# Kernel tuning notes

Measured on AMD Instinct MI355X. Metric: run time of the kernel, lower is better.

## Reference

```python
import jax, jax.numpy as jnp
import numpy as np

B, L, D = 4, 4096, 1024


def setup_inputs() -> dict:
    key = jax.random.key(0)
    ks = jax.random.split(key, 10)
    s = 1.0 / np.sqrt(D)  # torch Linear default init scale
    return {
        "x": jax.random.normal(ks[0], (B, L, D), dtype=jnp.float32),
        "hidden": jax.random.normal(ks[1], (B, D), dtype=jnp.float32),
        "W_ln_z": jax.random.uniform(ks[2], (D, D), jnp.float32, -s, s),
        "b_ln_z": jax.random.uniform(ks[3], (D,), jnp.float32, -s, s),
        "W_dt": jax.random.uniform(ks[4], (D, D), jnp.float32, -s, s),
        "b_dt": jax.random.uniform(ks[5], (D,), jnp.float32, -s, s),
        "W_y": jax.random.uniform(ks[6], (D, D), jnp.float32, -s, s),
        "b_y": jax.random.uniform(ks[7], (D,), jnp.float32, -s, s),
        "W_g": jax.random.uniform(ks[8], (D, D), jnp.float32, -s, s),
        "b_g": jax.random.uniform(ks[9], (D,), jnp.float32, -s, s),
    }


def reference(x, hidden, W_ln_z, b_ln_z, W_dt, b_dt, W_y, b_y, W_g, b_g):
    # Linear projections (torch Linear: x @ W.T + b)
    z_pre = x @ W_ln_z.T + b_ln_z          # (B, L, D)
    dt_pre = x @ W_dt.T + b_dt             # (B, L, D)

    # -softplus(-u) == log_sigmoid(u)
    ln_z = jax.nn.log_sigmoid(z_pre)       # ln z
    ln_da = jax.nn.log_sigmoid(dt_pre)     # ln(delta*a)
    ln_z_da = ln_z + ln_da
    ln_o_da = jax.nn.log_sigmoid(-dt_pre)  # -softplus(dt_pre)

    ln_o_da_cumsum = jnp.cumsum(ln_o_da, axis=1)
    # log-space parallel scan: h_t = sum_{s<=t} z_s*da_s * prod_{s<r<=t} o_da_r
    lcse = jax.lax.cumlogsumexp(ln_z_da - ln_o_da_cumsum, axis=1)
    h_inner = jnp.exp(lcse + ln_o_da_cumsum)                       # (B, L, D)
    h_cross = jnp.exp(ln_o_da_cumsum) * hidden[:, None, :]         # (B, L, D)
    h = h_inner + h_cross

    gate = jax.nn.silu(x @ W_g.T + b_g)
    y = (h @ W_y.T + b_y) * gate
    return y, h
```

## Files before the change

kernel.cpp:

```cpp
#include <hip/hip_runtime.h>


#define BDIM 4
#define LDIM 4096
#define DDIM 1024
#define MROWS (BDIM * LDIM)
#define KDIM 1024
#define NPROJ 3072
#define NCHUNK 64
#define LCHUNK 64

typedef __attribute__((ext_vector_type(8))) short short8v;
typedef __attribute__((ext_vector_type(4))) float f32x4;

__device__ __forceinline__ float bf2f(short u) {
    union { float f; unsigned int i; } v;
    v.i = ((unsigned int)(unsigned short)u) << 16;
    return v.f;
}
__device__ __forceinline__ short f2bf(float f) {
    union { float f; unsigned int i; } v; v.f = f;
    unsigned int r = v.i + 0x7FFFu + ((v.i >> 16) & 1u);
    return (short)(r >> 16);
}
__device__ __forceinline__ float sigf(float x) { return 1.f / (1.f + __expf(-x)); }

__global__ void cast_f32_bf16(const float* __restrict__ src, short* __restrict__ dst, int n4) {
    int i = blockIdx.x * blockDim.x + threadIdx.x;
    int stride = gridDim.x * blockDim.x;
    for (; i < n4; i += stride) {
        float4 v = reinterpret_cast<const float4*>(src)[i];
        short4 o;
        o.x = f2bf(v.x); o.y = f2bf(v.y); o.z = f2bf(v.z); o.w = f2bf(v.w);
        reinterpret_cast<short4*>(dst)[i] = o;
    }
}

__global__ void cast4_f32_bf16(const float* __restrict__ s0, const float* __restrict__ s1,
                               const float* __restrict__ s2, const float* __restrict__ s3,
                               short* __restrict__ dst) {
    int i = blockIdx.x * blockDim.x + threadIdx.x;
    int seg = i >> 18, off = i & ((1 << 18) - 1);
    const float* s = (seg == 0) ? s0 : (seg == 1) ? s1 : (seg == 2) ? s2 : s3;
    float4 v = reinterpret_cast<const float4*>(s)[off];
    short4 o;
    o.x = f2bf(v.x); o.y = f2bf(v.y); o.z = f2bf(v.z); o.w = f2bf(v.w);
    reinterpret_cast<short4*>(dst)[i] = o;
}


#define STAGE(arr, gbase, half, kofs)                                              \
  do {                                                                             \
    _Pragma("unroll")                                                              \
    for (int _i = 0; _i < 2; ++_i) {                                               \
      int _c = _i * 512 + tid;                                                     \
      int _row = _c >> 3, _g = _c & 7;                                             \
      int _gsw = _g ^ (_row & 7);                                                  \
      __builtin_amdgcn_global_load_lds(                                            \
        (const __attribute__((address_space(1))) void*)(                           \
            (gbase) + (size_t)((half) * 128 + _row) * K + (kofs) + _gsw * 8),      \
        (__attribute__((address_space(3))) void*)(                                 \
            &arr[(_i * 512 + wid * 64) * 8]),                                      \
        16, 0, 0);                                                                 \
    }                                                                              \
  } while (0)

#define LDA4(dst, arr)                                                             \
  _Pragma("unroll")                                                                \
  for (int _m = 0; _m < 4; ++_m) {                                                 \
    int _r = _m * 32 + wm * 16 + lrow;                                             \
    _Pragma("unroll")                                                              \
    for (int _kk = 0; _kk < 2; ++_kk)                                              \
      dst[_m][_kk] = *(const short8v*)&arr[_r * 64 +                               \
                       (((_kk * 4 + kq) ^ (lrow & 7)) * 8)];                       \
  }

#define LDB2(dst, arr)                                                             \
  _Pragma("unroll")                                                                \
  for (int _n = 0; _n < 2; ++_n) {                                                 \
    int _r = _n * 64 + wn * 16 + lrow;                                             \
    _Pragma("unroll")                                                              \
    for (int _kk = 0; _kk < 2; ++_kk)                                              \
      dst[_n][_kk] = *(const short8v*)&arr[_r * 64 +                               \
                       (((_kk * 4 + kq) ^ (lrow & 7)) * 8)];                       \
  }

#define MFMAQ(mi0, ni0, afr, bfr)                                                  \
  __builtin_amdgcn_s_setprio(1);                                                   \
  _Pragma("unroll")                                                                \
  for (int _kk = 0; _kk < 2; ++_kk)                                                \
    _Pragma("unroll")                                                              \
    for (int _m = 0; _m < 4; ++_m)                                                 \
      _Pragma("unroll")                                                            \
      for (int _n = 0; _n < 2; ++_n)                                               \
        acc[(mi0) + _m][(ni0) + _n] = __builtin_amdgcn_mfma_f32_16x16x32_bf16(     \
            afr[_m][_kk], bfr[_n][_kk], acc[(mi0) + _m][(ni0) + _n], 0, 0, 0);     \
  __builtin_amdgcn_s_setprio(0);

#define BARB()       __builtin_amdgcn_s_barrier()
#define BAR_VM4()    asm volatile("s_waitcnt vmcnt(4)\ns_barrier" ::: "memory")
#define BAR_VM0()    asm volatile("s_waitcnt vmcnt(0)\ns_barrier" ::: "memory")

template<int OUT_BF16, int HAS_GATE>
__global__ __launch_bounds__(512, 2) void gemm256(
    const short* __restrict__ A, const short* __restrict__ Bm,
    const float* __restrict__ bias, void* __restrict__ Cv,
    int M, int N, int K,
    const short* __restrict__ gate, int ldg)
{
    __shared__ short As0h0[8192], As0h1[8192], As1h0[8192], As1h1[8192];
    __shared__ short Bs0h0[8192], Bs0h1[8192], Bs1h0[8192], Bs1h1[8192];

    const int tid  = threadIdx.x;
    const int lane = tid & 63;
    const int wid  = tid >> 6;
    const int wm   = wid >> 2;
    const int wn   = wid & 3;
    const int lrow = lane & 15;
    const int kq   = lane >> 4;

    const int gx  = gridDim.x;
    const int nwg = gx * gridDim.y;
    int flat = blockIdx.y * gx + blockIdx.x;
    if ((nwg & 7) == 0) { int q = nwg >> 3; flat = (flat & 7) * q + (flat >> 3); }
    const int m0 = (flat / gx) * 256;
    const int n0 = (flat % gx) * 256;

    const short* Abase = A + (size_t)m0 * K;
    const short* Bbase = Bm + (size_t)n0 * K;

    f32x4 acc[8][4];
#pragma unroll
    for (int i = 0; i < 8; ++i)
#pragma unroll
        for (int j = 0; j < 4; ++j)
            acc[i][j] = (f32x4){0.f, 0.f, 0.f, 0.f};

    STAGE(As0h0, Abase, 0, 0);
    STAGE(As0h1, Abase, 1, 0);
    STAGE(Bs0h0, Bbase, 0, 0);
    STAGE(Bs0h1, Bbase, 1, 0);
    STAGE(As1h0, Abase, 0, 64);
    STAGE(Bs1h0, Bbase, 0, 64);
    BAR_VM4();

    const int NT = K / 64;
    for (int t = 0; t < NT; t += 2) {
        const int k1 = (t + 1) * 64, k2 = (t + 2) * 64, k3 = (t + 3) * 64;
        const bool more = (t + 2) < NT;
        short8v af[4][2], b0[2][2], b1[2][2];

        LDA4(af, As0h0) LDB2(b0, Bs0h0) LDB2(b1, Bs0h1)
        STAGE(As1h1, Abase, 1, k1);
        STAGE(Bs1h1, Bbase, 1, k1);
        BARB(); MFMAQ(0, 0, af, b0) MFMAQ(0, 2, af, b1) BARB();

        LDA4(af, As0h1)
        if (more) { STAGE(As0h0, Abase, 0, k2); STAGE(Bs0h0, Bbase, 0, k2); }
        BARB(); MFMAQ(4, 2, af, b1) MFMAQ(4, 0, af, b0)
        if (more) { BAR_VM4(); } else { BAR_VM0(); }

        LDA4(af, As1h0) LDB2(b0, Bs1h0) LDB2(b1, Bs1h1)
        if (more) { STAGE(As0h1, Abase, 1, k2); STAGE(Bs0h1, Bbase, 1, k2); }
        BARB(); MFMAQ(0, 0, af, b0) MFMAQ(0, 2, af, b1) BARB();

        LDA4(af, As1h1)
        if (more) { STAGE(As1h0, Abase, 0, k3); STAGE(Bs1h0, Bbase, 0, k3); }
        BARB(); MFMAQ(4, 2, af, b1) MFMAQ(4, 0, af, b0)
        if (more) { BAR_VM4(); } else { BARB(); }
    }

    const int lr4 = (lane >> 4) * 4;
#pragma unroll
    for (int mi = 0; mi < 8; ++mi) {
        int rowb = m0 + mi * 32 + wm * 16 + lr4;
#pragma unroll
        for (int ni = 0; ni < 4; ++ni) {
            int col = n0 + ni * 64 + wn * 16 + lrow;
            float bv = bias[col];
#pragma unroll
            for (int r = 0; r < 4; ++r) {
                int row = rowb + r;
                float val = acc[mi][ni][r] + bv;
                if (HAS_GATE) {
                    float g = bf2f(gate[(size_t)row * ldg + col]);
                    val *= g * sigf(g);
                }
                if (OUT_BF16)
                    ((short*)Cv)[(size_t)row * N + col] = f2bf(val);
                else
                    ((float*)Cv)[(size_t)row * N + col] = val;
            }
        }
    }
}

__global__ __launch_bounds__(1024) void chunk_reduce(
    const short* __restrict__ pre, float* __restrict__ sA, float* __restrict__ sBv)
{
    const int d = threadIdx.x;
    const int c = blockIdx.x;
    const int b = blockIdx.y;
    float Aacc = 1.f, Bacc = 0.f;
    size_t base = ((size_t)(b * LDIM) + c * LCHUNK) * NPROJ;
    for (int i = 0; i < LCHUNK; ++i) {
        float z  = bf2f(pre[base + d]);
        float dt = bf2f(pre[base + DDIM + d]);
        float e  = __expf(-dt);
        float r  = 1.f / (1.f + e);
        float oda = e * r;
        float zda = sigf(z) * r;
        Bacc = zda + oda * Bacc;
        Aacc *= oda;
        base += NPROJ;
    }
    int idx = ((b * NCHUNK + c) << 10) + d;
    sA[idx]  = Aacc;
    sBv[idx] = Bacc;
}

__global__ __launch_bounds__(1024) void chunk_prefix(
    const float* __restrict__ sA, const float* __restrict__ sBv,
    const float* __restrict__ hidden, float* __restrict__ sI)
{
    const int d = threadIdx.x;
    const int b = blockIdx.x;
    float h = hidden[b * DDIM + d];
    for (int c = 0; c < NCHUNK; ++c) {
        int idx = ((b * NCHUNK + c) << 10) + d;
        sI[idx] = h;
        h = sBv[idx] + sA[idx] * h;
    }
}

__global__ __launch_bounds__(1024) void chunk_apply(
    const short* __restrict__ pre, const float* __restrict__ sI,
    float* __restrict__ hout, short* __restrict__ hbf)
{
    const int d = threadIdx.x;
    const int c = blockIdx.x;
    const int b = blockIdx.y;
    float h = sI[((b * NCHUNK + c) << 10) + d];
    size_t base  = ((size_t)(b * LDIM) + c * LCHUNK) * NPROJ;
    size_t obase = ((size_t)(b * LDIM) + c * LCHUNK) * DDIM + d;
    for (int i = 0; i < LCHUNK; ++i) {
        float z  = bf2f(pre[base + d]);
        float dt = bf2f(pre[base + DDIM + d]);
        float e  = __expf(-dt);
        float r  = 1.f / (1.f + e);
        float oda = e * r;
        float zda = sigf(z) * r;
        h = zda + oda * h;
        hout[obase] = h;
        hbf[obase]  = f2bf(h);
        base += NPROJ;
        obase += DDIM;
    }
}

extern "C" void kernel_launch(void* const* d_in, const int* in_sizes, int n_in,
                              void* d_out, int out_size, void* d_ws, size_t ws_size,
                              hipStream_t stream) {
    const float* x      = (const float*)d_in[0];
    const float* hidden = (const float*)d_in[1];
    const float* W_ln_z = (const float*)d_in[2];
    const float* b_ln_z = (const float*)d_in[3];
    const float* W_dt   = (const float*)d_in[4];
    const float* b_dt   = (const float*)d_in[5];
    const float* W_y    = (const float*)d_in[6];
    const float* b_y    = (const float*)d_in[7];
    const float* W_g    = (const float*)d_in[8];
    const float* b_g    = (const float*)d_in[9];

    char* ws = (char*)d_ws;
    short* x_bf   = (short*)(ws + 0);
    short* Wcat   = (short*)(ws + 33554432);
    short* Wy_bf  = (short*)(ws + 39845888);
    float* biascat= (float*)(ws + 41943040);
    short* pre    = (short*)(ws + 41955328);
    float* sA     = (float*)(ws + 142618624);
    float* sBv    = (float*)(ws + 143667200);
    float* sI     = (float*)(ws + 144715776);

    cast_f32_bf16<<<2048, 256, 0, stream>>>(x, x_bf, (MROWS * KDIM) / 4);
    cast4_f32_bf16<<<4096, 256, 0, stream>>>(W_ln_z, W_dt, W_g, W_y, Wcat);

    hipMemcpyAsync(biascat,            b_ln_z, DDIM * sizeof(float), hipMemcpyDeviceToDevice, stream);
    hipMemcpyAsync(biascat + DDIM,     b_dt,   DDIM * sizeof(float), hipMemcpyDeviceToDevice, stream);
    hipMemcpyAsync(biascat + 2 * DDIM, b_g,    DDIM * sizeof(float), hipMemcpyDeviceToDevice, stream);

    gemm256<1, 0><<<dim3(NPROJ / 256, MROWS / 256), 512, 0, stream>>>(
        x_bf, Wcat, biascat, pre, MROWS, NPROJ, KDIM, nullptr, 0);

    float* y_out = (float*)d_out;
    float* h_out = (float*)d_out + (size_t)MROWS * DDIM;
    short* h_bf  = x_bf;
    chunk_reduce<<<dim3(NCHUNK, BDIM), 1024, 0, stream>>>(pre, sA, sBv);
    chunk_prefix<<<dim3(BDIM), 1024, 0, stream>>>(sA, sBv, hidden, sI);
    chunk_apply<<<dim3(NCHUNK, BDIM), 1024, 0, stream>>>(pre, sI, h_out, h_bf);

    gemm256<0, 1><<<dim3(DDIM / 256, MROWS / 256), 512, 0, stream>>>(
        h_bf, Wy_bf, b_y, y_out, MROWS, DDIM, KDIM, pre + 2 * DDIM, NPROJ);
}
```

Baseline: 281.1 us.

## Split GEMM phases into finer LDS/MFMA interleave and pack scan kernel elements

The GEMM main loop is split into eight smaller phases, each pairing one LDS fragment load and one global stage with a single MFMA quarter, separated by barriers. The vmcnt waits are issued separately from the barriers so global loads can overlap more MFMA work. Separately, the chunked scan kernels now process two channels per thread with 32-bit bf16 pair loads and float2 stores, halving the thread count. This adds barriers per iteration, and the scan kernels launch fewer threads, which lowers parallelism on an already small grid.

```diff
diff --git a/kernel.cpp b/kernel.cpp
--- a/kernel.cpp
+++ b/kernel.cpp
@@ -97,9 +97,9 @@
             afr[_m][_kk], bfr[_n][_kk], acc[(mi0) + _m][(ni0) + _n], 0, 0, 0);     \
   __builtin_amdgcn_s_setprio(0);
 
-#define BARB()       __builtin_amdgcn_s_barrier()
-#define BAR_VM4()    asm volatile("s_waitcnt vmcnt(4)\ns_barrier" ::: "memory")
-#define BAR_VM0()    asm volatile("s_waitcnt vmcnt(0)\ns_barrier" ::: "memory")
+#define BARB()   __builtin_amdgcn_s_barrier()
+#define VM4()    asm volatile("s_waitcnt vmcnt(4)")
+#define VM0()    asm volatile("s_waitcnt vmcnt(0)")
 
 template<int OUT_BF16, int HAS_GATE>
 __global__ __launch_bounds__(512, 2) void gemm256(
@@ -142,7 +142,7 @@
     STAGE(Bs0h1, Bbase, 1, 0);
     STAGE(As1h0, Abase, 0, 64);
     STAGE(Bs1h0, Bbase, 0, 64);
-    BAR_VM4();
+    VM4(); BARB();
 
     const int NT = K / 64;
     for (int t = 0; t < NT; t += 2) {
@@ -150,24 +150,35 @@
         const bool more = (t + 2) < NT;
         short8v af[4][2], b0[2][2], b1[2][2];
 
-        LDA4(af, As0h0) LDB2(b0, Bs0h0) LDB2(b1, Bs0h1)
+        LDA4(af, As0h0) LDB2(b0, Bs0h0)
         STAGE(As1h1, Abase, 1, k1);
+        BARB(); MFMAQ(0, 0, af, b0)
+
+        LDB2(b1, Bs0h1)
         STAGE(Bs1h1, Bbase, 1, k1);
-        BARB(); MFMAQ(0, 0, af, b0) MFMAQ(0, 2, af, b1) BARB();
+        BARB(); MFMAQ(0, 2, af, b1)
 
         LDA4(af, As0h1)
-        if (more) { STAGE(As0h0, Abase, 0, k2); STAGE(Bs0h0, Bbase, 0, k2); }
-        BARB(); MFMAQ(4, 2, af, b1) MFMAQ(4, 0, af, b0)
-        if (more) { BAR_VM4(); } else { BAR_VM0(); }
-
-        LDA4(af, As1h0) LDB2(b0, Bs1h0) LDB2(b1, Bs1h1)
-        if (more) { STAGE(As0h1, Abase, 1, k2); STAGE(Bs0h1, Bbase, 1, k2); }
-        BARB(); MFMAQ(0, 0, af, b0) MFMAQ(0, 2, af, b1) BARB();
+        if (more) STAGE(As0h0, Abase, 0, k2);
+        BARB(); MFMAQ(4, 2, af, b1)
+
+        if (more) { STAGE(Bs0h0, Bbase, 0, k2); VM4(); } else { VM0(); }
+        BARB(); MFMAQ(4, 0, af, b0)
+
+        LDA4(af, As1h0) LDB2(b0, Bs1h0)
+        if (more) STAGE(As0h1, Abase, 1, k2);
+        BARB(); MFMAQ(0, 0, af, b0)
+
+        LDB2(b1, Bs1h1)
+        if (more) STAGE(Bs0h1, Bbase, 1, k2);
+        BARB(); MFMAQ(0, 2, af, b1)
 
         LDA4(af, As1h1)
-        if (more) { STAGE(As1h0, Abase, 0, k3); STAGE(Bs1h0, Bbase, 0, k3); }
-        BARB(); MFMAQ(4, 2, af, b1) MFMAQ(4, 0, af, b0)
-        if (more) { BAR_VM4(); } else { BARB(); }
+        if (more) STAGE(As1h0, Abase, 0, k3);
+        BARB(); MFMAQ(4, 2, af, b1)
+
+        if (more) { STAGE(Bs1h0, Bbase, 0, k3); VM4(); }
+        BARB(); MFMAQ(4, 0, af, b0)
     }
 
     const int lr4 = (lane >> 4) * 4;
@@ -195,28 +206,28 @@
     }
 }
 
-__global__ __launch_bounds__(1024) void chunk_reduce(
+__global__ __launch_bounds__(512) void chunk_reduce(
     const short* __restrict__ pre, float* __restrict__ sA, float* __restrict__ sBv)
 {
-    const int d = threadIdx.x;
+    const int t = threadIdx.x;
     const int c = blockIdx.x;
     const int b = blockIdx.y;
-    float Aacc = 1.f, Bacc = 0.f;
+    float A0 = 1.f, A1 = 1.f, B0 = 0.f, B1 = 0.f;
     size_t base = ((size_t)(b * LDIM) + c * LCHUNK) * NPROJ;
     for (int i = 0; i < LCHUNK; ++i) {
-        float z  = bf2f(pre[base + d]);
-        float dt = bf2f(pre[base + DDIM + d]);
-        float e  = __expf(-dt);
-        float r  = 1.f / (1.f + e);
-        float oda = e * r;
-        float zda = sigf(z) * r;
-        Bacc = zda + oda * Bacc;
-        Aacc *= oda;
+        unsigned int zz = *reinterpret_cast<const unsigned int*>(&pre[base + 2 * t]);
+        unsigned int dd = *reinterpret_cast<const unsigned int*>(&pre[base + DDIM + 2 * t]);
+        float z0 = bf2f((short)(zz & 0xffff)), z1 = bf2f((short)(zz >> 16));
+        float d0 = bf2f((short)(dd & 0xffff)), d1 = bf2f((short)(dd >> 16));
+        float e0 = __expf(-d0), r0 = 1.f / (1.f + e0), o0 = e0 * r0, q0 = sigf(z0) * r0;
+        float e1 = __expf(-d1), r1 = 1.f / (1.f + e1), o1 = e1 * r1, q1 = sigf(z1) * r1;
+        B0 = q0 + o0 * B0; A0 *= o0;
+        B1 = q1 + o1 * B1; A1 *= o1;
         base += NPROJ;
     }
-    int idx = ((b * NCHUNK + c) << 10) + d;
-    sA[idx]  = Aacc;
-    sBv[idx] = Bacc;
+    int idx = ((b * NCHUNK + c) << 10) + 2 * t;
+    *reinterpret_cast<float2*>(&sA[idx])  = make_float2(A0, A1);
+    *reinterpret_cast<float2*>(&sBv[idx]) = make_float2(B0, B1);
 }
 
 __global__ __launch_bounds__(1024) void chunk_prefix(
@@ -233,26 +244,30 @@
     }
 }
 
-__global__ __launch_bounds__(1024) void chunk_apply(
+__global__ __launch_bounds__(512) void chunk_apply(
     const short* __restrict__ pre, const float* __restrict__ sI,
     float* __restrict__ hout, short* __restrict__ hbf)
 {
-    const int d = threadIdx.x;
+    const int t = threadIdx.x;
     const int c = blockIdx.x;
     const int b = blockIdx.y;
-    float h = sI[((b * NCHUNK + c) << 10) + d];
+    float2 hi = *reinterpret_cast<const float2*>(&sI[((b * NCHUNK + c) << 10) + 2 * t]);
+    float h0 = hi.x, h1 = hi.y;
     size_t base  = ((size_t)(b * LDIM) + c * LCHUNK) * NPROJ;
-    size_t obase = ((size_t)(b * LDIM) + c * LCHUNK) * DDIM + d;
+    size_t obase = ((size_t)(b * LDIM) + c * LCHUNK) * DDIM + 2 * t;
     for (int i = 0; i < LCHUNK; ++i) {
-        float z  = bf2f(pre[base + d]);
-        float dt = bf2f(pre[base + DDIM + d]);
-        float e  = __expf(-dt);
-        float r  = 1.f / (1.f + e);
-        float oda = e * r;
-        float zda = sigf(z) * r;
-        h = zda + oda * h;
-        hout[obase] = h;
-        hbf[obase]  = f2bf(h);
+        unsigned int zz = *reinterpret_cast<const unsigned int*>(&pre[base + 2 * t]);
+        unsigned int dd = *reinterpret_cast<const unsigned int*>(&pre[base + DDIM + 2 * t]);
+        float z0 = bf2f((short)(zz & 0xffff)), z1 = bf2f((short)(zz >> 16));
+        float d0 = bf2f((short)(dd & 0xffff)), d1 = bf2f((short)(dd >> 16));
+        float e0 = __expf(-d0), r0 = 1.f / (1.f + e0), o0 = e0 * r0, q0 = sigf(z0) * r0;
+        float e1 = __expf(-d1), r1 = 1.f / (1.f + e1), o1 = e1 * r1, q1 = sigf(z1) * r1;
+        h0 = q0 + o0 * h0;
+        h1 = q1 + o1 * h1;
+        *reinterpret_cast<float2*>(&hout[obase]) = make_float2(h0, h1);
+        unsigned int hp = ((unsigned int)(unsigned short)f2bf(h0)) |
+                          (((unsigned int)(unsigned short)f2bf(h1)) << 16);
+        *reinterpret_cast<unsigned int*>(&hbf[obase]) = hp;
         base += NPROJ;
         obase += DDIM;
     }
@@ -295,9 +310,9 @@
     float* y_out = (float*)d_out;
     float* h_out = (float*)d_out + (size_t)MROWS * DDIM;
     short* h_bf  = x_bf;
-    chunk_reduce<<<dim3(NCHUNK, BDIM), 1024, 0, stream>>>(pre, sA, sBv);
+    chunk_reduce<<<dim3(NCHUNK, BDIM), 512, 0, stream>>>(pre, sA, sBv);
     chunk_prefix<<<dim3(BDIM), 1024, 0, stream>>>(sA, sBv, hidden, sI);
-    chunk_apply<<<dim3(NCHUNK, BDIM), 1024, 0, stream>>>(pre, sI, h_out, h_bf);
+    chunk_apply<<<dim3(NCHUNK, BDIM), 512, 0, stream>>>(pre, sI, h_out, h_bf);
 
     gemm256<0, 1><<<dim3(DDIM / 256, MROWS / 256), 512, 0, stream>>>(
         h_bf, Wy_bf, b_y, y_out, MROWS, DDIM, KDIM, pre + 2 * DDIM, NPROJ);
```

Measured after the change: 264.8 us. 1.06x faster.
